# Performance work log

Hardware: AMD Instinct MI355X
Metric: run time of the kernel (lower is better)

## Reference

```python
import jax, jax.numpy as jnp
import numpy as np


def _conv3x3(x, w):
    # NCHW input, OIHW weight, stride 1, padding 1 (SAME for 3x3)
    return jax.lax.conv_general_dilated(
        x, w, window_strides=(1, 1), padding=((1, 1), (1, 1)),
        dimension_numbers=('NCHW', 'OIHW', 'NCHW'))


def _conv1x1(x, w):
    return jax.lax.conv_general_dilated(
        x, w, window_strides=(1, 1), padding=((0, 0), (0, 0)),
        dimension_numbers=('NCHW', 'OIHW', 'NCHW'))


def setup_inputs() -> dict:
    key = jax.random.key(0)
    k_x, k_w1, k_w2, k_wm = jax.random.split(key, 4)
    N, C, H, W = 16, 256, 64, 64
    fan = C * 9
    x = jax.random.normal(k_x, (N, C, H, W), dtype=jnp.float32)
    w1 = jax.random.normal(k_w1, (C, C, 3, 3), dtype=jnp.float32) * (2.0 / fan) ** 0.5
    w2 = jax.random.normal(k_w2, (C, C, 3, 3), dtype=jnp.float32) * (2.0 / fan) ** 0.5
    w_mask = jax.random.normal(k_wm, (1, C, 1, 1), dtype=jnp.float32) * (1.0 / C) ** 0.5
    b_mask = jnp.zeros((1,), dtype=jnp.float32)
    return {'x': x, 'w1': w1, 'w2': w2, 'w_mask': w_mask, 'b_mask': b_mask}


def reference(x, w1, w2, w_mask, b_mask):
    # MaskUnit: 1x1 conv -> logits -> hard binary mask (straight-through estimator)
    logits = _conv1x1(x, w_mask) + b_mask[None, :, None, None]  # [N,1,H,W]
    hard = (logits > 0).astype(x.dtype)
    mask = logits + jax.lax.stop_gradient(hard - logits)        # std mask, binary in fwd
    # dilated mask: 3x3 max-pool (covers 3x3 receptive field of active outputs)
    mask_dilate = jax.lax.reduce_window(
        mask, -jnp.inf, jax.lax.max, (1, 1, 3, 3), (1, 1, 1, 1), 'SAME')
    # sparse branch: conv1 gated by dilated mask, conv2 gated by std mask
    h = jax.nn.relu(_conv3x3(x, w1) * mask_dilate)
    h = jax.nn.relu(_conv3x3(h, w2) * mask)
    # apply_mask + residual (mask binary -> h*mask == h already, kept for fidelity)
    out = x + h * mask
    return out
```

## Files before the change

### kernel.cpp

```cpp
#include <hip/hip_runtime.h>
#include <hip/hip_bf16.h>

#define C_ 256
#define H_ 64
#define W_ 64
#define N_ 16
#define HW_ 4096
#define IMG_ (C_ * HW_)
#define PADIMG_ (66 * 66 * 256)
#define WT_ELEMS_ (9 * 256 * 256)

typedef short bf16x8 __attribute__((ext_vector_type(8)));
typedef float f32x4 __attribute__((ext_vector_type(4)));

__device__ __forceinline__ unsigned short f2bf(float f) {
  __hip_bfloat16 h = __float2bfloat16(f);
  return *reinterpret_cast<unsigned short*>(&h);
}

__device__ __forceinline__ void gld_lds16(const void* g, void* l) {
  __builtin_amdgcn_global_load_lds(
      (const __attribute__((address_space(1))) void*)g,
      (__attribute__((address_space(3))) void*)l, 16, 0, 0);
}

__global__ __launch_bounds__(256) void mask_kernel(
    const float* __restrict__ x, const float* __restrict__ wm,
    const float* __restrict__ bm, unsigned char* __restrict__ mask) {
  __shared__ float wms[C_];
  for (int i = threadIdx.x; i < C_; i += 256) wms[i] = wm[i];
  __syncthreads();
  int pix = blockIdx.x * 256 + threadIdx.x;
  int n = pix >> 12;
  int hw = pix & (HW_ - 1);
  const float* xp = x + (size_t)n * IMG_ + hw;
  double acc = (double)bm[0];
  for (int c = 0; c < C_; c++) acc += (double)xp[(size_t)c * HW_] * (double)wms[c];
  mask[pix] = (acc > 0.0) ? 1 : 0;
}

__global__ __launch_bounds__(256) void dilate_kernel(
    const unsigned char* __restrict__ mask, unsigned char* __restrict__ md) {
  int pix = blockIdx.x * 256 + threadIdx.x;
  int n = pix >> 12;
  int hw = pix & (HW_ - 1);
  int h = hw >> 6, w = hw & 63;
  int m = 0;
  for (int dy = -1; dy <= 1; dy++) {
    int hh = h + dy;
    if (hh < 0 || hh >= H_) continue;
    for (int dx = -1; dx <= 1; dx++) {
      int ww = w + dx;
      if (ww < 0 || ww >= W_) continue;
      m |= mask[n * HW_ + hh * W_ + ww];
    }
  }
  md[pix] = (unsigned char)m;
}

__global__ __launch_bounds__(256) void wt_kernel(
    const float* __restrict__ w1, const float* __restrict__ w2,
    short* __restrict__ Wt1, short* __restrict__ Wt2) {
  const int k = blockIdx.x, c = threadIdx.x;
  const float* src = blockIdx.y ? w2 : w1;
  short* dst = blockIdx.y ? Wt2 : Wt1;
  const float* s = src + ((size_t)k * 256 + c) * 9;
#pragma unroll
  for (int t = 0; t < 9; ++t)
    dst[t * 65536 + k * 256 + c] = (short)f2bf(s[t]);
}

__global__ __launch_bounds__(128) void halo_zero(short* __restrict__ Xp,
                                                 short* __restrict__ Hp) {
  int p = blockIdx.x;
  int r, c;
  if (p < 66) { r = 0; c = p; }
  else if (p < 132) { r = 65; c = p - 66; }
  else if (p < 196) { r = p - 131; c = 0; }
  else { r = p - 195; c = 65; }
  short* buf = blockIdx.z ? Hp : Xp;
  unsigned int* d = (unsigned int*)(buf + (size_t)blockIdx.y * PADIMG_ +
                                    (size_t)(r * 66 + c) * 256);
  d[threadIdx.x] = 0u;
}

__global__ __launch_bounds__(256) void xpad_kernel(
    const float* __restrict__ x, short* __restrict__ Xp) {
  __shared__ unsigned short lds[64 * 260];
  const int h = blockIdx.x, img = blockIdx.y;
  const int tid = threadIdx.x;
  const int wv = tid >> 6, wl = tid & 63;
  const float* xi = x + (size_t)img * IMG_ + h * 64;
#pragma unroll 4
  for (int i = 0; i < 64; ++i) {
    int c = i * 4 + wv;
    lds[wl * 260 + c] = f2bf(xi[(size_t)c * HW_ + wl]);
  }
  __syncthreads();
  short* Xpi = Xp + (size_t)img * PADIMG_ + ((h + 1) * 66 + 1) * 256;
#pragma unroll
  for (int j = 0; j < 16; ++j) {
    int w = j * 4 + wv;
    int c4 = wl * 4;
    uint2 d = *(const uint2*)&lds[w * 260 + c4];
    *(uint2*)&Xpi[(size_t)w * 256 + c4] = d;
  }
}

template <int EPI>
__global__ __launch_bounds__(256) void conv_mfma(
    const short* __restrict__ src, const short* __restrict__ Wt,
    const unsigned char* __restrict__ gate, const float* __restrict__ xres,
    short* __restrict__ dstH, float* __restrict__ dstF) {
  __shared__ short Wl[9 * 64 * 32];
  __shared__ short Bl[400 * 32];

  const int tid = threadIdx.x;
  const int lane = tid & 63, wave = tid >> 6;
  const int quad = lane >> 4, ln15 = lane & 15;
  const int ch0 = blockIdx.x * 64;
  const int h0 = blockIdx.y * 4;
  const int img = blockIdx.z;

  const int lr = lane >> 2;
  const int lc = (lane & 3) * 8;

  const short* Xbase = src + (size_t)img * PADIMG_ + (size_t)(h0 * 66) * 256;

  f32x4 acc[4][4];
#pragma unroll
  for (int i = 0; i < 4; ++i)
#pragma unroll
    for (int j = 0; j < 4; ++j) acc[i][j] = {0.f, 0.f, 0.f, 0.f};

  for (int kk = 0; kk < 8; ++kk) {
    const int ko = kk * 32;
    for (int n = wave; n < 25; n += 4) {
      gld_lds16(Xbase + (size_t)(n * 16 + lr) * 256 + ko + lc, Bl + n * 512);
    }
#pragma unroll
    for (int t = 0; t < 9; ++t) {
      gld_lds16(Wt + t * 65536 + (ch0 + wave * 16 + lr) * 256 + ko + lc,
                Wl + (t * 64 + wave * 16) * 32);
    }
    __syncthreads();

#pragma unroll
    for (int t = 0; t < 9; ++t) {
      const int dy = t / 3, dx = t % 3;
      bf16x8 a[4], b[4];
#pragma unroll
      for (int i = 0; i < 4; ++i)
        a[i] = *(const bf16x8*)&Wl[(t * 64 + i * 16 + ln15) * 32 + quad * 8];
#pragma unroll
      for (int j = 0; j < 4; ++j) {
        const int pl = (wave + dy) * 66 + j * 16 + ln15 + dx;
        b[j] = *(const bf16x8*)&Bl[pl * 32 + quad * 8];
      }
#pragma unroll
      for (int i = 0; i < 4; ++i)
#pragma unroll
        for (int j = 0; j < 4; ++j)
          acc[i][j] = __builtin_amdgcn_mfma_f32_16x16x32_bf16(a[i], b[j],
                                                              acc[i][j], 0, 0, 0);
    }
    __syncthreads();
  }

  const int r = h0 + wave;
#pragma unroll
  for (int j = 0; j < 4; ++j) {
    const int col = j * 16 + ln15;
    const int pidx = r * 64 + col;
    const unsigned char g = gate[img * HW_ + pidx];
#pragma unroll
    for (int i = 0; i < 4; ++i) {
      f32x4 v = acc[i][j];
      const int ch = ch0 + i * 16 + quad * 4;
      float e0 = g ? fmaxf(v[0], 0.f) : 0.f;
      float e1 = g ? fmaxf(v[1], 0.f) : 0.f;
      float e2 = g ? fmaxf(v[2], 0.f) : 0.f;
      float e3 = g ? fmaxf(v[3], 0.f) : 0.f;
      if (EPI == 0) {
        uint2 u;
        u.x = (unsigned int)f2bf(e0) | ((unsigned int)f2bf(e1) << 16);
        u.y = (unsigned int)f2bf(e2) | ((unsigned int)f2bf(e3) << 16);
        short* d = dstH + (size_t)img * PADIMG_ +
                   ((size_t)((r + 1) * 66 + (col + 1))) * 256 + ch;
        *(uint2*)d = u;
      } else {
        size_t o = (size_t)img * IMG_ + (size_t)ch * HW_ + pidx;
        dstF[o] = xres[o] + e0;
        dstF[o + HW_] = xres[o + HW_] + e1;
        dstF[o + 2 * HW_] = xres[o + 2 * HW_] + e2;
        dstF[o + 3 * HW_] = xres[o + 3 * HW_] + e3;
      }
    }
  }
}

extern "C" void kernel_launch(void* const* d_in, const int* in_sizes, int n_in,
                              void* d_out, int out_size, void* d_ws,
                              size_t ws_size, hipStream_t stream) {
  const float* x = (const float*)d_in[0];
  const float* w1 = (const float*)d_in[1];
  const float* w2 = (const float*)d_in[2];
  const float* wmask = (const float*)d_in[3];
  const float* bmask = (const float*)d_in[4];
  float* out = (float*)d_out;

  char* ws = (char*)d_ws;
  unsigned char* mask = (unsigned char*)ws;
  unsigned char* md = (unsigned char*)(ws + 65536);
  short* Wt1 = (short*)(ws + 131072);
  short* Wt2 = Wt1 + WT_ELEMS_;
  short* Xp = (short*)(ws + 2490368);

  const size_t fixed = 2490368;
  const size_t tailpad = 16384;
  const size_t per_img = 2 * (size_t)PADIMG_ * 2;
  int B = (ws_size > fixed + tailpad)
              ? (int)((ws_size - fixed - tailpad) / per_img) : 0;
  if (B > N_) B = N_;
  if (B < 1) B = 1;
  short* Hp = Xp + (size_t)B * PADIMG_;

  wt_kernel<<<dim3(256, 2), 256, 0, stream>>>(w1, w2, Wt1, Wt2);
  mask_kernel<<<256, 256, 0, stream>>>(x, wmask, bmask, mask);
  dilate_kernel<<<256, 256, 0, stream>>>(mask, md);
  halo_zero<<<dim3(260, B, 2), 128, 0, stream>>>(Xp, Hp);

  for (int n0 = 0; n0 < N_; n0 += B) {
    const int nb = (N_ - n0 < B) ? (N_ - n0) : B;
    xpad_kernel<<<dim3(64, nb), 256, 0, stream>>>(x + (size_t)n0 * IMG_, Xp);
    conv_mfma<0><<<dim3(4, 16, nb), 256, 0, stream>>>(
        Xp, Wt1, md + n0 * HW_, nullptr, Hp, nullptr);
    conv_mfma<1><<<dim3(4, 16, nb), 256, 0, stream>>>(
        Hp, Wt2, mask + n0 * HW_, x + (size_t)n0 * IMG_, nullptr,
        out + (size_t)n0 * IMG_);
  }
}
```

Baseline: 322.7 us.

## Fuse mask into xpad, double conv row tile, read weights from global

The mask logit computation moves into the bf16 pad/transpose kernel, so x is read once for both jobs. Dilation now runs per image batch. The conv kernel processes 8 rows per block instead of 4, doubling the accumulator tile to 4x8 MFMA tiles. It drops the LDS staging of weights in favour of direct global loads of A fragments, and adds launch_bounds with 2 blocks per CU. This trades more register pressure and uncached global weight reads for fewer blocks and less redundant input halo loading.

After: 469.8 us. 1.46x slower.

```diff
diff --git a/kernel.cpp b/kernel.cpp
--- a/kernel.cpp
+++ b/kernel.cpp
@@ -24,19 +24,42 @@
       (__attribute__((address_space(3))) void*)l, 16, 0, 0);
 }
 
-__global__ __launch_bounds__(256) void mask_kernel(
+__global__ __launch_bounds__(256) void xpadmask_kernel(
     const float* __restrict__ x, const float* __restrict__ wm,
-    const float* __restrict__ bm, unsigned char* __restrict__ mask) {
-  __shared__ float wms[C_];
-  for (int i = threadIdx.x; i < C_; i += 256) wms[i] = wm[i];
+    const float* __restrict__ bm, short* __restrict__ Xp,
+    unsigned char* __restrict__ mask) {
+  __shared__ unsigned short lds[64 * 260];
+  __shared__ float wms[256];
+  __shared__ double sums[4][64];
+  const int h = blockIdx.x, img = blockIdx.y;
+  const int tid = threadIdx.x;
+  const int wv = tid >> 6, wl = tid & 63;
+  wms[tid] = wm[tid];
   __syncthreads();
-  int pix = blockIdx.x * 256 + threadIdx.x;
-  int n = pix >> 12;
-  int hw = pix & (HW_ - 1);
-  const float* xp = x + (size_t)n * IMG_ + hw;
-  double acc = (double)bm[0];
-  for (int c = 0; c < C_; c++) acc += (double)xp[(size_t)c * HW_] * (double)wms[c];
-  mask[pix] = (acc > 0.0) ? 1 : 0;
+  const float* xi = x + (size_t)img * IMG_ + h * 64;
+  double acc = 0.0;
+#pragma unroll 4
+  for (int i = 0; i < 64; ++i) {
+    int c = i * 4 + wv;
+    float v = xi[(size_t)c * HW_ + wl];
+    lds[wl * 260 + c] = f2bf(v);
+    acc += (double)v * (double)wms[c];
+  }
+  sums[wv][wl] = acc;
+  __syncthreads();
+  short* Xpi = Xp + (size_t)img * PADIMG_ + ((h + 1) * 66 + 1) * 256;
+#pragma unroll
+  for (int j = 0; j < 16; ++j) {
+    int w = j * 4 + wv;
+    int c4 = wl * 4;
+    uint2 d = *(const uint2*)&lds[w * 260 + c4];
+    *(uint2*)&Xpi[(size_t)w * 256 + c4] = d;
+  }
+  if (wv == 0) {
+    double t = sums[0][wl] + sums[1][wl] + sums[2][wl] + sums[3][wl] +
+               (double)bm[0];
+    mask[img * HW_ + h * 64 + wl] = (t > 0.0) ? 1 : 0;
+  }
 }
 
 __global__ __launch_bounds__(256) void dilate_kernel(
@@ -84,93 +107,66 @@
   d[threadIdx.x] = 0u;
 }
 
-__global__ __launch_bounds__(256) void xpad_kernel(
-    const float* __restrict__ x, short* __restrict__ Xp) {
-  __shared__ unsigned short lds[64 * 260];
-  const int h = blockIdx.x, img = blockIdx.y;
-  const int tid = threadIdx.x;
-  const int wv = tid >> 6, wl = tid & 63;
-  const float* xi = x + (size_t)img * IMG_ + h * 64;
-#pragma unroll 4
-  for (int i = 0; i < 64; ++i) {
-    int c = i * 4 + wv;
-    lds[wl * 260 + c] = f2bf(xi[(size_t)c * HW_ + wl]);
-  }
-  __syncthreads();
-  short* Xpi = Xp + (size_t)img * PADIMG_ + ((h + 1) * 66 + 1) * 256;
-#pragma unroll
-  for (int j = 0; j < 16; ++j) {
-    int w = j * 4 + wv;
-    int c4 = wl * 4;
-    uint2 d = *(const uint2*)&lds[w * 260 + c4];
-    *(uint2*)&Xpi[(size_t)w * 256 + c4] = d;
-  }
-}
-
 template <int EPI>
-__global__ __launch_bounds__(256) void conv_mfma(
+__global__ __launch_bounds__(256, 2) void conv_mfma(
     const short* __restrict__ src, const short* __restrict__ Wt,
     const unsigned char* __restrict__ gate, const float* __restrict__ xres,
     short* __restrict__ dstH, float* __restrict__ dstF) {
-  __shared__ short Wl[9 * 64 * 32];
-  __shared__ short Bl[400 * 32];
+  __shared__ short Bl[672 * 32];
 
   const int tid = threadIdx.x;
   const int lane = tid & 63, wave = tid >> 6;
   const int quad = lane >> 4, ln15 = lane & 15;
   const int ch0 = blockIdx.x * 64;
-  const int h0 = blockIdx.y * 4;
+  const int h0 = blockIdx.y * 8;
   const int img = blockIdx.z;
 
   const int lr = lane >> 2;
   const int lc = (lane & 3) * 8;
 
   const short* Xbase = src + (size_t)img * PADIMG_ + (size_t)(h0 * 66) * 256;
-
-  f32x4 acc[4][4];
+  const short* Abase = Wt + (size_t)(ch0 + ln15) * 256 + quad * 8;
+
+  f32x4 acc[4][8];
 #pragma unroll
   for (int i = 0; i < 4; ++i)
 #pragma unroll
-    for (int j = 0; j < 4; ++j) acc[i][j] = {0.f, 0.f, 0.f, 0.f};
+    for (int j = 0; j < 8; ++j) acc[i][j] = {0.f, 0.f, 0.f, 0.f};
 
   for (int kk = 0; kk < 8; ++kk) {
     const int ko = kk * 32;
-    for (int n = wave; n < 25; n += 4) {
+    for (int n = wave; n < 42; n += 4) {
       gld_lds16(Xbase + (size_t)(n * 16 + lr) * 256 + ko + lc, Bl + n * 512);
-    }
-#pragma unroll
-    for (int t = 0; t < 9; ++t) {
-      gld_lds16(Wt + t * 65536 + (ch0 + wave * 16 + lr) * 256 + ko + lc,
-                Wl + (t * 64 + wave * 16) * 32);
     }
     __syncthreads();
 
 #pragma unroll
     for (int t = 0; t < 9; ++t) {
       const int dy = t / 3, dx = t % 3;
-      bf16x8 a[4], b[4];
+      bf16x8 a[4], b[8];
 #pragma unroll
       for (int i = 0; i < 4; ++i)
-        a[i] = *(const bf16x8*)&Wl[(t * 64 + i * 16 + ln15) * 32 + quad * 8];
-#pragma unroll
-      for (int j = 0; j < 4; ++j) {
-        const int pl = (wave + dy) * 66 + j * 16 + ln15 + dx;
+        a[i] = *(const bf16x8*)(Abase + (size_t)(t * 256 + i * 16) * 256 + ko);
+#pragma unroll
+      for (int j = 0; j < 8; ++j) {
+        const int pl = (wave * 2 + (j >> 2) + dy) * 66 + (j & 3) * 16 + ln15 + dx;
         b[j] = *(const bf16x8*)&Bl[pl * 32 + quad * 8];
       }
 #pragma unroll
       for (int i = 0; i < 4; ++i)
 #pragma unroll
-        for (int j = 0; j < 4; ++j)
+        for (int j = 0; j < 8; ++j)
           acc[i][j] = __builtin_amdgcn_mfma_f32_16x16x32_bf16(a[i], b[j],
                                                               acc[i][j], 0, 0, 0);
     }
     __syncthreads();
   }
 
-  const int r = h0 + wave;
-#pragma unroll
-  for (int j = 0; j < 4; ++j) {
-    const int col = j * 16 + ln15;
+  const int rbase = h0 + wave * 2;
+#pragma unroll
+  for (int j = 0; j < 8; ++j) {
+    const int r = rbase + (j >> 2);
+    const int col = (j & 3) * 16 + ln15;
     const int pidx = r * 64 + col;
     const unsigned char g = gate[img * HW_ + pidx];
 #pragma unroll
@@ -217,7 +213,7 @@
   short* Xp = (short*)(ws + 2490368);
 
   const size_t fixed = 2490368;
-  const size_t tailpad = 16384;
+  const size_t tailpad = 32768;
   const size_t per_img = 2 * (size_t)PADIMG_ * 2;
   int B = (ws_size > fixed + tailpad)
               ? (int)((ws_size - fixed - tailpad) / per_img) : 0;
@@ -226,16 +222,17 @@
   short* Hp = Xp + (size_t)B * PADIMG_;
 
   wt_kernel<<<dim3(256, 2), 256, 0, stream>>>(w1, w2, Wt1, Wt2);
-  mask_kernel<<<256, 256, 0, stream>>>(x, wmask, bmask, mask);
-  dilate_kernel<<<256, 256, 0, stream>>>(mask, md);
   halo_zero<<<dim3(260, B, 2), 128, 0, stream>>>(Xp, Hp);
 
   for (int n0 = 0; n0 < N_; n0 += B) {
     const int nb = (N_ - n0 < B) ? (N_ - n0) : B;
-    xpad_kernel<<<dim3(64, nb), 256, 0, stream>>>(x + (size_t)n0 * IMG_, Xp);
-    conv_mfma<0><<<dim3(4, 16, nb), 256, 0, stream>>>(
+    xpadmask_kernel<<<dim3(64, nb), 256, 0, stream>>>(
+        x + (size_t)n0 * IMG_, wmask, bmask, Xp, mask + n0 * HW_);
+    dilate_kernel<<<nb * HW_ / 256, 256, 0, stream>>>(mask + n0 * HW_,
+                                                      md + n0 * HW_);
+    conv_mfma<0><<<dim3(4, 8, nb), 256, 0, stream>>>(
         Xp, Wt1, md + n0 * HW_, nullptr, Hp, nullptr);
-    conv_mfma<1><<<dim3(4, 16, nb), 256, 0, stream>>>(
+    conv_mfma<1><<<dim3(4, 8, nb), 256, 0, stream>>>(
         Hp, Wt2, mask + n0 * HW_, x + (size_t)n0 * IMG_, nullptr,
         out + (size_t)n0 * IMG_);
   }
```
